# Kernel tuning notes

Hardware: AMD Instinct MI355X
Metric: run time of the kernel (lower is better)

## Reference

```python
import math
import jax, jax.numpy as jnp
import numpy as np


def setup_inputs() -> dict:
    key = jax.random.key(0)
    k1, k2, k3, k4 = jax.random.split(key, 4)
    B, K, D = 131072, 64, 8
    NC = D * (D + 1) // 2  # 36
    pi = jax.random.uniform(k1, (B, K), dtype=jnp.float32)
    mu = jax.random.normal(k2, (K, D), dtype=jnp.float32)
    # 'ALREADY CONSTRAINED' Cholesky entries: keep them positive (uniform),
    # +0.1 offset keeps diagonal safely away from 0 for the log.
    L_constrained = jax.random.uniform(k3, (K, NC), dtype=jnp.float32) + 0.1
    target = jax.random.normal(k4, (B, D), dtype=jnp.float32)
    return {"pi": pi, "mu": mu, "L_constrained": L_constrained, "target": target}


def reference(pi, mu, L_constrained, target):
    B, K = pi.shape
    D = mu.shape[1]
    norm_const = -0.5 * D * math.log(2.0 * math.pi)
    ti, tj = np.tril_indices(D)
    # scatter packed cholesky into dense lower-triangular (K, D, D)
    L = jnp.zeros((K, D, D), dtype=target.dtype).at[:, ti, tj].set(L_constrained)
    diff = target[:, None, :] - mu[None, :, :]          # (B, K, D)
    # batch over components, treat B as multiple RHS: L (K,D,D) @ z = b (K,D,B)
    b = jnp.transpose(diff, (1, 2, 0))                   # (K, D, B)
    z = jax.scipy.linalg.solve_triangular(L, b, lower=True)  # (K, D, B)
    M = jnp.sum(z * z, axis=1)                           # (K, B) Mahalanobis^2
    log_dets = jnp.sum(jnp.log(jnp.diagonal(L, axis1=-2, axis2=-1)), axis=-1)  # (K,)
    log_probs = norm_const - log_dets[:, None] - 0.5 * M  # (K, B)
    weighted = log_probs.T + jnp.log(pi + 1e-10)          # (B, K)
    nll = -jnp.mean(jax.scipy.special.logsumexp(weighted, axis=1))
    return nll
```

## Files before the change

kernel.cpp:

```cpp
#include <hip/hip_runtime.h>
#include <math.h>

#define B_TOTAL 131072
#define K_COMP  64
#define D_DIM   8
#define NC      36
#define NFEAT   96
#define ROWS_PB 128
#define RT_PW   2

#define NORM_CONST (-7.3515082656373815f)

typedef __attribute__((ext_vector_type(8))) short bf16x8;
typedef __attribute__((ext_vector_type(4))) float f32x4;

static __device__ __forceinline__ unsigned short bf16_rne(float x) {
    unsigned u = __float_as_uint(x);
    u += 0x7FFF + ((u >> 16) & 1);
    return (unsigned short)(u >> 16);
}
static __device__ __forceinline__ float bf16_f32(unsigned short h) {
    return __uint_as_float(((unsigned)h) << 16);
}

__global__ void mdn_precompute(const float* __restrict__ mu,
                               const float* __restrict__ Lc,
                               unsigned short* __restrict__ psi_hi,
                               unsigned short* __restrict__ psi_lo,
                               float* __restrict__ out) {
    int k = threadIdx.x;
    if (k == 0) out[0] = 0.0f;
    if (k >= K_COMP) return;
    const float* Lk = Lc + k * NC;

    float L[D_DIM][D_DIM];
    float W[D_DIM][D_DIM];
#pragma unroll
    for (int i = 0; i < D_DIM; i++)
#pragma unroll
        for (int j = 0; j < D_DIM; j++) { L[i][j] = 0.0f; W[i][j] = 0.0f; }

    float logdet = 0.0f;
    int idx = 0;
#pragma unroll
    for (int i = 0; i < D_DIM; i++)
#pragma unroll
        for (int j = 0; j <= i; j++) {
            float v = Lk[idx++];
            L[i][j] = v;
            if (j == i) logdet += logf(v);
        }

#pragma unroll
    for (int j = 0; j < D_DIM; j++) {
        W[j][j] = 1.0f / L[j][j];
#pragma unroll
        for (int i = 0; i < D_DIM; i++) {
            if (i > j) {
                float acc = 0.0f;
#pragma unroll
                for (int m = 0; m < D_DIM; m++)
                    if (m >= j && m < i) acc += L[i][m] * W[m][j];
                W[i][j] = -acc / L[i][i];
            }
        }
    }

    float P[D_DIM][D_DIM];
#pragma unroll
    for (int a = 0; a < D_DIM; a++)
#pragma unroll
        for (int b = 0; b < D_DIM; b++) {
            float acc = 0.0f;
#pragma unroll
            for (int m = 0; m < D_DIM; m++) acc += W[m][a] * W[m][b];
            P[a][b] = acc;
        }

    float h[D_DIM];
    float qf = 0.0f;
#pragma unroll
    for (int i = 0; i < D_DIM; i++) {
        float acc = 0.0f;
#pragma unroll
        for (int j = 0; j < D_DIM; j++) acc += P[i][j] * mu[k * D_DIM + j];
        h[i] = acc;
        qf += mu[k * D_DIM + i] * acc;
    }
    float g = NORM_CONST - logdet - 0.5f * qf;

    float psi[NFEAT];
#pragma unroll
    for (int e = 0; e < NFEAT; e++) psi[e] = 0.0f;
#pragma unroll
    for (int a = 0; a < D_DIM; a++)
#pragma unroll
        for (int b = 0; b < D_DIM; b++) psi[8 * a + b] = -0.5f * P[a][b];
#pragma unroll
    for (int b = 0; b < D_DIM; b++) psi[64 + b] = h[b];
    psi[72] = g;

    unsigned short* oh = psi_hi + k * NFEAT;
    unsigned short* ol = psi_lo + k * NFEAT;
#pragma unroll
    for (int e = 0; e < NFEAT; e++) {
        unsigned short hi = bf16_rne(psi[e]);
        oh[e] = hi;
        ol[e] = bf16_rne(psi[e] - bf16_f32(hi));
    }
}

__global__ __launch_bounds__(256, 4) void mdn_main(
        const float* __restrict__ pi,
        const unsigned short* __restrict__ psi_hi,
        const unsigned short* __restrict__ psi_lo,
        const float* __restrict__ target,
        float* __restrict__ out) {
    const int tid = threadIdx.x;
    const int lane = tid & 63;
    const int w = tid >> 6;
    const int q = lane >> 4;
    const int n = lane & 15;
    const int rowbase = blockIdx.x * ROWS_PB;

    __shared__ float Tl[ROWS_PB * D_DIM];
    {
        const float4* src = (const float4*)(target + (size_t)rowbase * D_DIM);
        ((float4*)Tl)[tid] = src[tid];
    }
    __syncthreads();

    float lacc = 0.0f;

#pragma unroll
    for (int r = 0; r < RT_PW; r++) {
        const int row0 = (w * RT_PW + r) * 16;

        const float4* trow = (const float4*)(Tl + (row0 + n) * D_DIM);
        float4 tlo = trow[0], thi = trow[1];
        float tv[D_DIM] = {tlo.x, tlo.y, tlo.z, tlo.w, thi.x, thi.y, thi.z, thi.w};

        float pv[4][4];
#pragma unroll
        for (int reg = 0; reg < 4; reg++) {
            const float* pr = pi + (size_t)(rowbase + row0 + 4 * q + reg) * K_COMP + n;
#pragma unroll
            for (int nt = 0; nt < 4; nt++) pv[reg][nt] = pr[16 * nt];
        }

        float ta0 = (q & 2) ? ((q & 1) ? tlo.w : tlo.z) : ((q & 1) ? tlo.y : tlo.x);
        float ta1 = (q & 2) ? ((q & 1) ? thi.w : thi.z) : ((q & 1) ? thi.y : thi.x);

        bf16x8 Ahi[3], Alo[3];
#pragma unroll
        for (int j = 0; j < D_DIM; j++) {
            float f0 = ta0 * tv[j];
            unsigned short h0 = bf16_rne(f0);
            Ahi[0][j] = (short)h0;
            Alo[0][j] = (short)bf16_rne(f0 - bf16_f32(h0));

            float f1 = ta1 * tv[j];
            unsigned short h1 = bf16_rne(f1);
            Ahi[1][j] = (short)h1;
            Alo[1][j] = (short)bf16_rne(f1 - bf16_f32(h1));

            float f2 = (q == 0) ? tv[j] : ((q == 1 && j == 0) ? 1.0f : 0.0f);
            unsigned short h2 = bf16_rne(f2);
            Ahi[2][j] = (short)h2;
            Alo[2][j] = (short)bf16_rne(f2 - bf16_f32(h2));
        }

        f32x4 acc[4];
#pragma unroll
        for (int nt = 0; nt < 4; nt++) {
            const unsigned short* bh = psi_hi + ((16 * nt + n) * NFEAT + 8 * q);
            const unsigned short* bl = psi_lo + ((16 * nt + n) * NFEAT + 8 * q);
            f32x4 a = {0.0f, 0.0f, 0.0f, 0.0f};
#pragma unroll
            for (int ks = 0; ks < 3; ks++) {
                bf16x8 Bh = *(const bf16x8*)(bh + 32 * ks);
                bf16x8 Bl = *(const bf16x8*)(bl + 32 * ks);
                a = __builtin_amdgcn_mfma_f32_16x16x32_bf16(Ahi[ks], Bh, a, 0, 0, 0);
                a = __builtin_amdgcn_mfma_f32_16x16x32_bf16(Alo[ks], Bh, a, 0, 0, 0);
                a = __builtin_amdgcn_mfma_f32_16x16x32_bf16(Ahi[ks], Bl, a, 0, 0, 0);
            }
            acc[nt] = a;
        }

#pragma unroll
        for (int reg = 0; reg < 4; reg++) {
            float c0 = acc[0][reg], c1 = acc[1][reg], c2 = acc[2][reg], c3 = acc[3][reg];
            float mrow = fmaxf(fmaxf(c0, c1), fmaxf(c2, c3));
#pragma unroll
            for (int off = 1; off < 16; off <<= 1)
                mrow = fmaxf(mrow, __shfl_xor(mrow, off));
            float s = (pv[reg][0] + 1e-10f) * __expf(c0 - mrow)
                    + (pv[reg][1] + 1e-10f) * __expf(c1 - mrow)
                    + (pv[reg][2] + 1e-10f) * __expf(c2 - mrow)
                    + (pv[reg][3] + 1e-10f) * __expf(c3 - mrow);
#pragma unroll
            for (int off = 1; off < 16; off <<= 1)
                s += __shfl_xor(s, off);
            float lse = mrow + __logf(s);
            lacc += (n == 0) ? lse : 0.0f;
        }
    }

#pragma unroll
    for (int off = 32; off > 0; off >>= 1) lacc += __shfl_down(lacc, off);
    __shared__ float wsum[4];
    if (lane == 0) wsum[w] = lacc;
    __syncthreads();
    if (tid == 0) {
        atomicAdd(out, (wsum[0] + wsum[1] + wsum[2] + wsum[3]) * (-1.0f / (float)B_TOTAL));
    }
}

extern "C" void kernel_launch(void* const* d_in, const int* in_sizes, int n_in,
                              void* d_out, int out_size, void* d_ws, size_t ws_size,
                              hipStream_t stream) {
    const float* pi  = (const float*)d_in[0];
    const float* mu  = (const float*)d_in[1];
    const float* Lc  = (const float*)d_in[2];
    const float* tgt = (const float*)d_in[3];
    float* out = (float*)d_out;

    unsigned short* psi_hi = (unsigned short*)d_ws;
    unsigned short* psi_lo = (unsigned short*)((char*)d_ws + K_COMP * NFEAT * 2);

    mdn_precompute<<<1, 64, 0, stream>>>(mu, Lc, psi_hi, psi_lo, out);
    mdn_main<<<B_TOTAL / ROWS_PB, 256, 0, stream>>>(pi, psi_hi, psi_lo, tgt, out);
}
```

Before: 99.61 us.

## Swap MFMA operand roles so psi stays in registers, and vectorize pi loads

The matmul is transposed: psi coefficients become the A operand and are loaded once per thread into registers, instead of being re-read from global memory for every row tile. Target features become the B operand, so each lane holds all 64 components' logits for a single row. That lets pi be read as contiguous float4 vectors and cuts the logsumexp reduction to two cross-lane shuffles instead of four. Block size doubles to 256 rows with 4 tiles per wave and launch bounds drop to 2 blocks per SM, which raises register use and lowers occupancy in exchange for reusing psi across more rows.

```diff
diff --git a/kernel.cpp b/kernel.cpp
--- a/kernel.cpp
+++ b/kernel.cpp
@@ -6,8 +6,8 @@
 #define D_DIM   8
 #define NC      36
 #define NFEAT   96
-#define ROWS_PB 128
-#define RT_PW   2
+#define ROWS_PB 256
+#define RT_PW   4
 
 #define NORM_CONST (-7.3515082656373815f)
 
@@ -110,7 +110,7 @@
     }
 }
 
-__global__ __launch_bounds__(256, 4) void mdn_main(
+__global__ __launch_bounds__(256, 2) void mdn_main(
         const float* __restrict__ pi,
         const unsigned short* __restrict__ psi_hi,
         const unsigned short* __restrict__ psi_lo,
@@ -126,84 +126,95 @@
     __shared__ float Tl[ROWS_PB * D_DIM];
     {
         const float4* src = (const float4*)(target + (size_t)rowbase * D_DIM);
-        ((float4*)Tl)[tid] = src[tid];
-    }
+        float4* dst = (float4*)Tl;
+        dst[tid] = src[tid];
+        dst[tid + 256] = src[tid + 256];
+    }
+
+    bf16x8 Ah[4][3], Al[4][3];
+#pragma unroll
+    for (int mt = 0; mt < 4; mt++)
+#pragma unroll
+        for (int ks = 0; ks < 3; ks++) {
+            const int off = (16 * mt + n) * NFEAT + 32 * ks + 8 * q;
+            Ah[mt][ks] = *(const bf16x8*)(psi_hi + off);
+            Al[mt][ks] = *(const bf16x8*)(psi_lo + off);
+        }
+
     __syncthreads();
 
     float lacc = 0.0f;
 
-#pragma unroll
+#pragma unroll 2
     for (int r = 0; r < RT_PW; r++) {
-        const int row0 = (w * RT_PW + r) * 16;
-
-        const float4* trow = (const float4*)(Tl + (row0 + n) * D_DIM);
-        float4 tlo = trow[0], thi = trow[1];
-        float tv[D_DIM] = {tlo.x, tlo.y, tlo.z, tlo.w, thi.x, thi.y, thi.z, thi.w};
-
-        float pv[4][4];
-#pragma unroll
-        for (int reg = 0; reg < 4; reg++) {
-            const float* pr = pi + (size_t)(rowbase + row0 + 4 * q + reg) * K_COMP + n;
-#pragma unroll
-            for (int nt = 0; nt < 4; nt++) pv[reg][nt] = pr[16 * nt];
-        }
-
-        float ta0 = (q & 2) ? ((q & 1) ? tlo.w : tlo.z) : ((q & 1) ? tlo.y : tlo.x);
-        float ta1 = (q & 2) ? ((q & 1) ? thi.w : thi.z) : ((q & 1) ? thi.y : thi.x);
-
-        bf16x8 Ahi[3], Alo[3];
+        const int row0 = w * (RT_PW * 16) + r * 16;
+        const int grow = rowbase + row0 + n;
+
+        f32x4 pv4[4];
+#pragma unroll
+        for (int mt = 0; mt < 4; mt++)
+            pv4[mt] = *(const f32x4*)(pi + (size_t)grow * K_COMP + 16 * mt + 4 * q);
+
+        const f32x4* trow = (const f32x4*)(Tl + (row0 + n) * D_DIM);
+        f32x4 tlo = trow[0], thi = trow[1];
+        float tv[D_DIM] = {tlo[0], tlo[1], tlo[2], tlo[3],
+                           thi[0], thi[1], thi[2], thi[3]};
+
+        float ta0 = (q & 2) ? ((q & 1) ? tlo[3] : tlo[2]) : ((q & 1) ? tlo[1] : tlo[0]);
+        float ta1 = (q & 2) ? ((q & 1) ? thi[3] : thi[2]) : ((q & 1) ? thi[1] : thi[0]);
+
+        bf16x8 Bh[3], Bl[3];
 #pragma unroll
         for (int j = 0; j < D_DIM; j++) {
             float f0 = ta0 * tv[j];
             unsigned short h0 = bf16_rne(f0);
-            Ahi[0][j] = (short)h0;
-            Alo[0][j] = (short)bf16_rne(f0 - bf16_f32(h0));
+            Bh[0][j] = (short)h0;
+            Bl[0][j] = (short)bf16_rne(f0 - bf16_f32(h0));
 
             float f1 = ta1 * tv[j];
             unsigned short h1 = bf16_rne(f1);
-            Ahi[1][j] = (short)h1;
-            Alo[1][j] = (short)bf16_rne(f1 - bf16_f32(h1));
+            Bh[1][j] = (short)h1;
+            Bl[1][j] = (short)bf16_rne(f1 - bf16_f32(h1));
 
             float f2 = (q == 0) ? tv[j] : ((q == 1 && j == 0) ? 1.0f : 0.0f);
             unsigned short h2 = bf16_rne(f2);
-            Ahi[2][j] = (short)h2;
-            Alo[2][j] = (short)bf16_rne(f2 - bf16_f32(h2));
+            Bh[2][j] = (short)h2;
+            Bl[2][j] = (short)bf16_rne(f2 - bf16_f32(h2));
         }
 
         f32x4 acc[4];
 #pragma unroll
-        for (int nt = 0; nt < 4; nt++) {
-            const unsigned short* bh = psi_hi + ((16 * nt + n) * NFEAT + 8 * q);
-            const unsigned short* bl = psi_lo + ((16 * nt + n) * NFEAT + 8 * q);
+        for (int mt = 0; mt < 4; mt++) {
             f32x4 a = {0.0f, 0.0f, 0.0f, 0.0f};
 #pragma unroll
             for (int ks = 0; ks < 3; ks++) {
-                bf16x8 Bh = *(const bf16x8*)(bh + 32 * ks);
-                bf16x8 Bl = *(const bf16x8*)(bl + 32 * ks);
-                a = __builtin_amdgcn_mfma_f32_16x16x32_bf16(Ahi[ks], Bh, a, 0, 0, 0);
-                a = __builtin_amdgcn_mfma_f32_16x16x32_bf16(Alo[ks], Bh, a, 0, 0, 0);
-                a = __builtin_amdgcn_mfma_f32_16x16x32_bf16(Ahi[ks], Bl, a, 0, 0, 0);
+                a = __builtin_amdgcn_mfma_f32_16x16x32_bf16(Ah[mt][ks], Bh[ks], a, 0, 0, 0);
+                a = __builtin_amdgcn_mfma_f32_16x16x32_bf16(Al[mt][ks], Bh[ks], a, 0, 0, 0);
+                a = __builtin_amdgcn_mfma_f32_16x16x32_bf16(Ah[mt][ks], Bl[ks], a, 0, 0, 0);
             }
-            acc[nt] = a;
-        }
-
-#pragma unroll
-        for (int reg = 0; reg < 4; reg++) {
-            float c0 = acc[0][reg], c1 = acc[1][reg], c2 = acc[2][reg], c3 = acc[3][reg];
-            float mrow = fmaxf(fmaxf(c0, c1), fmaxf(c2, c3));
-#pragma unroll
-            for (int off = 1; off < 16; off <<= 1)
-                mrow = fmaxf(mrow, __shfl_xor(mrow, off));
-            float s = (pv[reg][0] + 1e-10f) * __expf(c0 - mrow)
-                    + (pv[reg][1] + 1e-10f) * __expf(c1 - mrow)
-                    + (pv[reg][2] + 1e-10f) * __expf(c2 - mrow)
-                    + (pv[reg][3] + 1e-10f) * __expf(c3 - mrow);
-#pragma unroll
-            for (int off = 1; off < 16; off <<= 1)
-                s += __shfl_xor(s, off);
-            float lse = mrow + __logf(s);
-            lacc += (n == 0) ? lse : 0.0f;
-        }
+            acc[mt] = a;
+        }
+
+        float m0 = fmaxf(fmaxf(acc[0][0], acc[0][1]), fmaxf(acc[0][2], acc[0][3]));
+        float m1 = fmaxf(fmaxf(acc[1][0], acc[1][1]), fmaxf(acc[1][2], acc[1][3]));
+        float m2 = fmaxf(fmaxf(acc[2][0], acc[2][1]), fmaxf(acc[2][2], acc[2][3]));
+        float m3 = fmaxf(fmaxf(acc[3][0], acc[3][1]), fmaxf(acc[3][2], acc[3][3]));
+        float mrow = fmaxf(fmaxf(m0, m1), fmaxf(m2, m3));
+        mrow = fmaxf(mrow, __shfl_xor(mrow, 16));
+        mrow = fmaxf(mrow, __shfl_xor(mrow, 32));
+
+        float s = 0.0f;
+#pragma unroll
+        for (int mt = 0; mt < 4; mt++) {
+            s += (pv4[mt][0] + 1e-10f) * __expf(acc[mt][0] - mrow);
+            s += (pv4[mt][1] + 1e-10f) * __expf(acc[mt][1] - mrow);
+            s += (pv4[mt][2] + 1e-10f) * __expf(acc[mt][2] - mrow);
+            s += (pv4[mt][3] + 1e-10f) * __expf(acc[mt][3] - mrow);
+        }
+        s += __shfl_xor(s, 16);
+        s += __shfl_xor(s, 32);
+
+        if (q == 0) lacc += mrow + __logf(s);
     }
 
 #pragma unroll
```

Measured after the change: 93.54 us. 6.1% less time.
